# Optimization experiments

Measured on AMD Instinct MI355X. Metric: run time of the kernel, lower is better.

Reference implementation:

```python
import jax, jax.numpy as jnp
import numpy as np

V = 131072          # total vertices (hits) across all events
K = 64              # neighbours per vertex, col 0 == self
NSEG = 4            # number of events (row splits segments)
THRESHOLD = 0.5     # hierarchy score cut (layer's non-trainable threshold var)


def setup_inputs() -> dict:
    key = jax.random.key(0)
    k1, k2 = jax.random.split(key)
    score = jax.random.uniform(k1, (V, 1), dtype=jnp.float32)
    seg = V // NSEG
    base = (jnp.arange(V, dtype=jnp.int32) // seg) * seg
    # random neighbours constrained to the same segment; column 0 is self
    rnd = jax.random.randint(k2, (V, K - 1), 0, seg, dtype=jnp.int32) + base[:, None]
    nidxs = jnp.concatenate([jnp.arange(V, dtype=jnp.int32)[:, None], rnd], axis=1)
    row_splits = (jnp.arange(NSEG + 1, dtype=jnp.int32) * seg)
    return {"score": score, "nidxs": nidxs, "row_splits": row_splits}


def _local_group(score1, nidxs, row_splits, thr):
    """Greedy threshold-based neighbour grouping (HGCalML LocalGroup op).

    Vertices are visited per segment in descending score order. An unused
    vertex becomes a group seed; if its score > thr it absorbs all of its
    not-yet-used neighbours. Returns fixed-shape (-1 padded) outputs so the
    whole thing is jit-compatible.
    """
    V_, K_ = nidxs.shape
    seg_id = jnp.searchsorted(row_splits, jnp.arange(V_, dtype=row_splits.dtype),
                              side='right') - 1
    # per-segment descending-score order == tf.argsort(DESC) per row split
    order = jnp.lexsort((-score1, seg_id)).astype(jnp.int32)
    kcols = jnp.arange(K_)

    def step(state, v):
        used, assign, dirn, sel, seed, count = state
        is_new = jnp.logical_not(used[v])                 # v not grouped yet -> seed
        expand = score1[v] > thr                          # absorb neighbours?
        cand = jnp.where(expand, nidxs[v],
                         jnp.where(kcols == 0, v, -1))    # else only self
        safe = jnp.clip(cand, 0, V_ - 1)
        valid = (cand >= 0) & jnp.logical_not(used[safe]) & is_new
        used = used.at[safe].set(used[safe] | valid)
        assign = assign.at[safe].set(jnp.where(valid, count, assign[safe]))
        dirn = dirn.at[v].set(jnp.where(valid, cand, -1))
        sel = sel.at[count].set(jnp.where(is_new, v, sel[count]))
        seed = seed.at[v].set(seed[v] | is_new)
        count = count + is_new.astype(jnp.int32)
        return (used, assign, dirn, sel, seed, count), None

    init = (jnp.zeros(V_, dtype=bool),                 # used
            jnp.full(V_, -1, jnp.int32),               # backgather: seed rank per vertex
            jnp.full((V_, K_), -1, jnp.int32),         # directed neighbour idxs
            jnp.full(V_, -1, jnp.int32),               # selected seed vertices, -1 padded
            jnp.zeros(V_, dtype=bool),                 # seed mask
            jnp.int32(0))
    (used, assign, dirn, sel, seed, count), _ = jax.lax.scan(step, init, order)
    cs0 = jnp.concatenate([jnp.zeros(1, jnp.int32),
                           jnp.cumsum(seed.astype(jnp.int32))])
    rs_new = cs0[row_splits]                           # new row splits over seeds
    return rs_new, dirn, sel[:, None], assign, count


def reference(score, nidxs, row_splits):
    # layer: score = clip(score, 0, 1); per-segment argsort; LocalGroup
    score1 = jnp.clip(score.reshape(-1), 0.0, 1.0)
    rs_new, dirnidx, sel, backgather, n_sel = _local_group(score1, nidxs,
                                                           row_splits, THRESHOLD)
    # return_backscatter=True -> back = [V, sel]; we return sel (padded) + n_sel
    # outputs: directed nidx (V,K), selection idxs (V,1 padded with -1),
    #          backgather (V,), new row splits, number selected
    return dirnidx, sel, backgather, rs_new, n_sel
```

## Files before the change

kernel.cpp:

```cpp
#include <hip/hip_runtime.h>
#include <stdint.h>

#define INFU 0xFFFFFFFFu
#define LCAP 32768
#define NC 128

__global__ void __launch_bounds__(256) k_hist(const float* score, unsigned* bcnt,
                                              unsigned* claim, int* sel, int V, int SEGN){
  int v = blockIdx.x*blockDim.x+threadIdx.x; if (v>=V) return;
  claim[v]=INFU;
  sel[v]=-1;
  float s = score[v]; s = fminf(fmaxf(s,0.f),1.f);
  int b = (int)(s*(float)SEGN); if (b>=SEGN) b=SEGN-1; if (b<0) b=0;
  int bd = SEGN-1-b;
  int seg = v / SEGN;
  atomicAdd(&bcnt[(size_t)seg*SEGN+bd], 1u);
}

__global__ void __launch_bounds__(1024) k_scan(const unsigned* in, const unsigned* claim,
                                               unsigned* outExcl, unsigned* segTotal,
                                               int SEGN, int mode){
  int seg = blockIdx.x; int tid = threadIdx.x; int lane = tid&63, wv = tid>>6;
  __shared__ unsigned wsum[16];
  const int CH = (SEGN+1023)>>10;
  int i0 = tid*CH, i1 = i0+CH; if (i1>SEGN) i1=SEGN;
  const size_t base = (size_t)seg*SEGN;
  unsigned sum=0;
  for (int i=i0;i<i1;i++){
    unsigned x = (mode==0)? in[base+i] : ((claim[base+i]==INFU)?1u:0u);
    sum+=x;
  }
  unsigned incl=sum;
  for (int off=1;off<64;off<<=1){ unsigned t=__shfl_up(incl,(unsigned)off); if (lane>=off) incl+=t; }
  if (lane==63) wsum[wv]=incl;
  __syncthreads();
  unsigned wbase=0,total=0;
  for (int w=0;w<16;w++){ unsigned s=wsum[w]; if (w<wv) wbase+=s; total+=s; }
  unsigned run = wbase + incl - sum;
  for (int i=i0;i<i1;i++){
    unsigned x = (mode==0)? in[base+i] : ((claim[base+i]==INFU)?1u:0u);
    outExcl[base+i]=run; run+=x;
  }
  if (tid==0 && segTotal) segTotal[seg]=total;
}

__global__ void __launch_bounds__(256) k_scatter(const float* score, const unsigned* bbase,
                                                 unsigned* bfill, unsigned long long* slot,
                                                 int V, int SEGN){
  int v = blockIdx.x*blockDim.x+threadIdx.x; if (v>=V) return;
  float s = score[v]; s=fminf(fmaxf(s,0.f),1.f);
  int b=(int)(s*(float)SEGN); if(b>=SEGN)b=SEGN-1; if(b<0)b=0;
  int bd=SEGN-1-b; int seg=v/SEGN;
  size_t bk = (size_t)seg*SEGN+bd;
  unsigned pos = bbase[bk] + atomicAdd(&bfill[bk],1u);
  unsigned kb = ~__float_as_uint(s);
  slot[(size_t)seg*SEGN+pos] = ((unsigned long long)kb<<32) | (unsigned)v;
}

__global__ void __launch_bounds__(256) k_bsort(const unsigned* bcnt, const unsigned* bbase,
                                               unsigned long long* slot, int V, int SEGN){
  int t = blockIdx.x*blockDim.x+threadIdx.x; if (t>=V) return;
  unsigned n = bcnt[t];
  if (n<2) return;
  int seg = t / SEGN;
  unsigned long long* a = slot + (size_t)seg*SEGN + bbase[t];
  for (unsigned i=1;i<n;i++){
    unsigned long long key=a[i]; int j=(int)i-1;
    while (j>=0 && a[j]>key){ a[j+1]=a[j]; j--; }
    a[j+1]=key;
  }
}

__global__ void __launch_bounds__(256) k_build(const unsigned long long* slot,
                                               int* ord, unsigned* rnkv, int* segE,
                                               int V, int SEGN){
  int r = blockIdx.x*blockDim.x+threadIdx.x; if (r>=V) return;
  unsigned long long sl = slot[r];
  int v = (int)(unsigned)(sl & 0xFFFFFFFFull);
  ord[r]=v;
  int seg = r / SEGN; int rl = r - seg*SEGN;
  rnkv[v] = (unsigned)rl;
  float s = __uint_as_float(~(unsigned)(sl>>32));
  bool ex = (s > 0.5f);
  if (rl==0 && !ex) segE[seg]=0;
  if (ex){
    if (rl==SEGN-1) segE[seg]=SEGN;
    else {
      float s2 = __uint_as_float(~(unsigned)(slot[r+1]>>32));
      if (!(s2 > 0.5f)) segE[seg]=rl+1;
    }
  }
}

__global__ void __launch_bounds__(256) k_pack4(const int* ord, const unsigned* rnkv, const int* nidxs,
                                               const int* segE, unsigned short* nbr16,
                                               int V, int K, int SEGN){
  const int K4 = K>>2;
  long long q = (long long)blockIdx.x*256 + threadIdx.x;
  if (q >= (long long)V*K4) return;
  int gr = (int)(q / K4); int k4 = (int)(q - (long long)gr*K4);
  int seg = gr / SEGN, r = gr - seg*SEGN;
  if (r >= segE[seg]) return;
  int v = ord[gr];
  const int4 nn = *(const int4*)(nidxs + (size_t)v*K + (size_t)k4*4);
  ushort4 o;
  o.x=(unsigned short)rnkv[nn.x]; o.y=(unsigned short)rnkv[nn.y];
  o.z=(unsigned short)rnkv[nn.z]; o.w=(unsigned short)rnkv[nn.w];
  *(ushort4*)(nbr16 + (size_t)gr*K + (size_t)k4*4) = o;
}
__global__ void __launch_bounds__(256) k_pack(const int* ord, const unsigned* rnkv, const int* nidxs,
                                              const int* segE, unsigned short* nbr16,
                                              int V, int K, int SEGN){
  long long t = (long long)blockIdx.x*256 + threadIdx.x;
  if (t >= (long long)V*K) return;
  int gr = (int)(t / K); int k = (int)(t - (long long)gr*K);
  int seg = gr / SEGN, r = gr - seg*SEGN;
  if (r >= segE[seg]) return;
  int v = ord[gr];
  int w = nidxs[(size_t)v*K + k];
  nbr16[t] = (unsigned short)rnkv[w];
}

__global__ void __launch_bounds__(1024) k_greedy(const unsigned short* nbr16, const int* ord,
                                                 const int* segE,
                                                 unsigned* claim, unsigned* srank,
                                                 unsigned* segTotal, unsigned* absorb,
                                                 int SEGN, int K){
  __shared__ unsigned s_cl[LCAP/2];
  __shared__ unsigned char s_pos[LCAP];
  __shared__ unsigned s_cand[NC];
  __shared__ unsigned long long s_McLo[NC];
  __shared__ unsigned long long s_McHi[NC];
  __shared__ unsigned long long s_anyLo, s_anyHi;
  __shared__ unsigned long long s_bm[16];
  __shared__ unsigned s_ws[16];
  __shared__ unsigned s_base;
  __shared__ unsigned s_wcur;
  __shared__ unsigned long long s_v0, s_v1;
  const int seg = blockIdx.x, tid = threadIdx.x, lane = tid&63, wv = tid>>6;
  unsigned* clg = claim + (size_t)seg*SEGN;
  const size_t segbase = (size_t)seg*SEGN;
  const int E = segE[seg];
  const int cap = (LCAP < SEGN) ? LCAP : SEGN;
  const int capw = (cap+1)>>1;
  for (int i=tid; i<capw; i+=1024) s_cl[i]=0xFFFFFFFFu;
  for (int i=tid; i<((cap+3)>>2); i+=1024) ((unsigned*)s_pos)[i]=0u;
  if (tid<NC) s_cand[tid]=INFU;
  const unsigned long long lt_mask = (lane==0) ? 0ull : ((~0ull) >> (64-lane));
  unsigned wcursor = 0;
  for (;;){
    __syncthreads();
    if (tid<NC){
      unsigned pc = s_cand[tid];
      if (pc!=INFU && pc<(unsigned)cap) s_pos[pc]=0;
      s_cand[tid]=INFU; s_McLo[tid]=0ull; s_McHi[tid]=0ull;
    }
    if (tid==NC)   s_anyLo=0ull;
    if (tid==NC+1) s_anyHi=0ull;
    int found = 0;
    for (;;){
      unsigned r = wcursor + (unsigned)(wv*64 + lane);
      bool undec=false;
      if (r<(unsigned)E){
        if (r<(unsigned)cap)
          undec = (((s_cl[r>>1]>>((r&1)*16))&0xFFFFu)==0xFFFFu);
        else
          undec = (__hip_atomic_load(&clg[r], __ATOMIC_RELAXED, __HIP_MEMORY_SCOPE_AGENT)==INFU);
      }
      unsigned long long m = __ballot(undec);
      if (lane==0) s_bm[wv]=m;
      __syncthreads();
      unsigned long long mb = (lane<16)? s_bm[lane] : 0ull;
      int pc16 = (int)__popcll(mb);
      int incl = pc16;
      #pragma unroll
      for (int off=1; off<16; off<<=1){ int t=__shfl_up(incl,off); if (lane>=off) incl+=t; }
      int total = __shfl(incl, 15);
      int below = __shfl(incl, wv) - __shfl(pc16, wv);
      int pos = found + below + (int)__popcll(m & lt_mask);
      if (undec && pos<NC){
        s_cand[pos]=r;
        if (r<(unsigned)cap) s_pos[r]=(unsigned char)(pos+1);
      }
      if (undec && pos==NC-1) s_wcur=r+1;
      bool filled = (found+total>=NC);
      bool winend = (wcursor + 1024 >= (unsigned)E);
      __syncthreads();
      if (filled){ wcursor = s_wcur; found=NC; break; }
      found += total;
      if (winend){ wcursor=(unsigned)E; break; }
      wcursor += 1024;
    }
    const int ncand = found;
    if (!ncand) break;
    unsigned rwq[8], cq[8];
    #pragma unroll
    for (int q=0;q<8;q++){
      int c=(wv<<3)|q;
      cq[q] = (c<ncand) ? s_cand[c] : INFU;
    }
    #pragma unroll
    for (int q=0;q<8;q++){
      rwq[q]=INFU;
      if (cq[q]!=INFU && lane<K)
        rwq[q] = (unsigned)nbr16[(segbase + cq[q])*K + lane];
    }
    const bool fastmap = (s_cand[ncand-1] < (unsigned)cap);
    #pragma unroll
    for (int q=0;q<8;q++){
      int c=(wv<<3)|q;
      if (cq[q]!=INFU){
        unsigned rw = rwq[q];
        int p = -1;
        if (fastmap){
          if (rw<(unsigned)cap){ p = (int)s_pos[rw] - 1; }
        } else {
          int pp=0;
          if (s_cand[pp+64]<=rw) pp+=64;
          if (s_cand[pp+32]<=rw) pp+=32;
          if (s_cand[pp+16]<=rw) pp+=16;
          if (s_cand[pp+8 ]<=rw) pp+=8;
          if (s_cand[pp+4 ]<=rw) pp+=4;
          if (s_cand[pp+2 ]<=rw) pp+=2;
          if (s_cand[pp+1 ]<=rw) pp+=1;
          if (pp<ncand && s_cand[pp]==rw) p=pp;
        }
        if (lane<K && p>c){
          if (p<64){ atomicOr(&s_McLo[c], 1ull<<p);      atomicOr(&s_anyLo, 1ull<<p); }
          else     { atomicOr(&s_McHi[c], 1ull<<(p-64)); atomicOr(&s_anyHi, 1ull<<(p-64)); }
        }
      }
    }
    __syncthreads();
    if (wv==0){
      const int n0 = (ncand<64)? ncand : 64;
      const int n1 = ncand - n0;
      const unsigned long long nmask0 = (n0==64)? ~0ull : ((1ull<<n0)-1ull);
      unsigned long long Mj0 = s_McLo[lane];
      unsigned long long any0 = s_anyLo & nmask0;
      unsigned long long valid0 = (~any0) & nmask0;
      unsigned long long rem = any0;
      while (rem){
        int i=__builtin_ctzll(rem); rem &= rem-1;
        bool pred = ((valid0>>lane)&1ull) && (lane<i) && ((Mj0>>i)&1ull);
        if (__ballot(pred)==0ull) valid0 |= (1ull<<i);
      }
      unsigned long long valid1 = 0ull;
      if (n1>0){
        const unsigned long long nmask1 = (n1==64)? ~0ull : ((1ull<<n1)-1ull);
        unsigned long long sp = ((valid0>>lane)&1ull) ? s_McHi[lane] : 0ull;
        #pragma unroll
        for (int off=32; off; off>>=1)
          sp |= (unsigned long long)__shfl_xor((long long)sp, off);
        unsigned long long Mj1 = s_McHi[64+lane];
        unsigned long long any1 = s_anyHi & nmask1;
        valid1 = (~(any1|sp)) & nmask1;
        unsigned long long rem1 = any1 & ~sp;
        while (rem1){
          int i=__builtin_ctzll(rem1); rem1 &= rem1-1;
          bool pred = ((valid1>>lane)&1ull) && (lane<i) && ((Mj1>>i)&1ull);
          if (__ballot(pred)==0ull) valid1 |= (1ull<<i);
        }
      }
      if (lane==0){ s_v0=valid0; s_v1=valid1; }
    }
    __syncthreads();
    const unsigned long long v0 = s_v0, v1 = s_v1;
    #pragma unroll
    for (int q=0;q<8;q++){
      int c=(wv<<3)|q;
      bool isv = (c<64) ? (((v0>>c)&1ull)!=0ull) : (((v1>>(c-64))&1ull)!=0ull);
      if (cq[q]!=INFU && isv){
        unsigned rw=rwq[q], cr=cq[q];
        if (rw>cr && rw!=INFU){
          if (rw<(unsigned)cap){
            unsigned idx=rw>>1, sh=(rw&1)*16;
            unsigned old=s_cl[idx];
            for(;;){
              unsigned curv=(old>>sh)&0xFFFFu;
              if (cr>=curv) break;
              unsigned neu=(old & ~(0xFFFFu<<sh)) | (cr<<sh);
              unsigned prev=atomicCAS(&s_cl[idx], old, neu);
              if (prev==old) break;
              old=prev;
            }
          } else {
            atomicMin(&clg[rw], cr);
          }
        }
      }
    }
  }
  __syncthreads();
  if (cap == SEGN){
    if (tid==0) s_base=0;
    __syncthreads();
    for (int p=0; p<cap; p+=1024){
      int i = p + tid;
      bool live = (i<cap);
      unsigned c16 = 0xFFFFu;
      if (live) c16 = (s_cl[i>>1]>>((i&1)*16))&0xFFFFu;
      bool isSeed = live && (c16==0xFFFFu);
      unsigned long long m = __ballot(isSeed);
      if (lane==0) s_ws[wv]=(unsigned)__popcll(m);
      __syncthreads();
      unsigned wbase=0, tot=0;
      for (int w2=0;w2<16;w2++){ unsigned t2=s_ws[w2]; if (w2<wv) wbase+=t2; tot+=t2; }
      unsigned ex = s_base + wbase + (unsigned)__popcll(m & lt_mask);
      if (live){
        srank[segbase + i] = ex;
        clg[i] = isSeed ? INFU : c16;
        absorb[ord[segbase + i]] = isSeed ? (unsigned)i : c16;
      }
      __syncthreads();
      if (tid==0) s_base += tot;
    }
    __syncthreads();
    if (tid==0) segTotal[seg] = s_base;
  } else {
    for (int r=tid; r<cap; r+=1024){
      unsigned c=(s_cl[r>>1]>>((r&1)*16))&0xFFFFu;
      clg[r] = (c==0xFFFFu) ? INFU : c;
    }
  }
}

__global__ void __launch_bounds__(256) k_absorb(const unsigned* rnkv, const unsigned* claim,
                                                unsigned* absorb, int V, int SEGN){
  int v = blockIdx.x*blockDim.x+threadIdx.x; if (v>=V) return;
  int seg = v / SEGN;
  unsigned r = rnkv[v];
  unsigned c = claim[(size_t)seg*SEGN + r];
  absorb[v] = (c==INFU)? r : c;
}

__global__ void __launch_bounds__(256) k_dirnAll4(const int* nidxs, const unsigned* rnkv,
                                                  const unsigned* absorb, const float* score,
                                                  const unsigned* segTotal,
                                                  const unsigned* srank,
                                                  int* dirn, int* sel, int* backg,
                                                  int* rs, int* nsel,
                                                  int V, int K, int SEGN, int NSEG){
  const int K4 = K>>2;
  long long q = (long long)blockIdx.x*256 + threadIdx.x;
  if (q >= (long long)V*K4) return;
  int v = (int)(q / K4); int k4 = (int)(q - (long long)v*K4);
  int seg = v / SEGN;
  if (q <= (long long)NSEG){
    unsigned run=0;
    for (int s=0;s<(int)q;s++) run+=segTotal[s];
    rs[q]=(int)run;
    if ((int)q==NSEG) nsel[0]=(int)run;
  }
  unsigned r = rnkv[v];
  unsigned a_self = absorb[v];
  bool seed = (a_self == r);
  if (k4==0){
    unsigned segOff=0;
    for (int s=0;s<seg;s++) segOff+=segTotal[s];
    unsigned g = segOff + srank[(size_t)seg*SEGN + a_self];
    backg[v] = (int)g;
    if (seed) sel[g] = v;
  }
  int4 o = make_int4(-1,-1,-1,-1);
  if (seed){
    float s = score[v]; s=fminf(fmaxf(s,0.f),1.f);
    if (!(s > 0.5f)){
      if (k4==0) o.x = v;
    } else {
      const int4 nn = *(const int4*)(nidxs + (size_t)v*K + (size_t)k4*4);
      if (absorb[nn.x]==r) o.x=nn.x;
      if (absorb[nn.y]==r) o.y=nn.y;
      if (absorb[nn.z]==r) o.z=nn.z;
      if (absorb[nn.w]==r) o.w=nn.w;
    }
  }
  *(int4*)(dirn + (size_t)v*K + (size_t)k4*4) = o;
}
__global__ void __launch_bounds__(256) k_dirnAll(const int* nidxs, const unsigned* rnkv,
                                                 const unsigned* absorb, const float* score,
                                                 const unsigned* segTotal,
                                                 const unsigned* srank,
                                                 int* dirn, int* sel, int* backg,
                                                 int* rs, int* nsel,
                                                 int V, int K, int SEGN, int NSEG){
  long long t = (long long)blockIdx.x*blockDim.x + threadIdx.x;
  if (t >= (long long)V*K) return;
  int v = (int)(t / K); int j = (int)(t - (long long)v*K);
  int seg = v / SEGN;
  if (t <= (long long)NSEG){
    unsigned run=0;
    for (int s=0;s<(int)t;s++) run+=segTotal[s];
    rs[t]=(int)run;
    if ((int)t==NSEG) nsel[0]=(int)run;
  }
  unsigned r = rnkv[v];
  unsigned a_self = absorb[v];
  bool seed = (a_self == r);
  if (j==0){
    unsigned segOff=0;
    for (int s=0;s<seg;s++) segOff+=segTotal[s];
    unsigned g = segOff + srank[(size_t)seg*SEGN + a_self];
    backg[v] = (int)g;
    if (seed) sel[g] = v;
  }
  int out = -1;
  if (seed){
    float s = score[v]; s=fminf(fmaxf(s,0.f),1.f);
    if (!(s > 0.5f)){
      out = (j==0)? v : -1;
    } else {
      int w = nidxs[(size_t)v*K + j];
      out = (absorb[w] == r)? w : -1;
    }
  }
  dirn[t] = out;
}

extern "C" void kernel_launch(void* const* d_in, const int* in_sizes, int n_in,
                              void* d_out, int out_size, void* d_ws, size_t ws_size,
                              hipStream_t stream) {
  const float* score   = (const float*)d_in[0];
  const int*   nidxs   = (const int*)d_in[1];
  (void)d_in[2];

  const int V    = in_sizes[0];
  const int K    = in_sizes[1] / V;
  const int NSEG = in_sizes[2] - 1;
  const int SEGN = V / NSEG;

  char* w = (char*)d_ws;
  unsigned long long* slot = (unsigned long long*)w;  w += (size_t)V*8;
  unsigned* bcnt  = (unsigned*)w; w += (size_t)V*4;
  unsigned* bfill = (unsigned*)w; w += (size_t)V*4;
  unsigned* bbase = (unsigned*)w; w += (size_t)V*4;
  int*      ord   = (int*)w;      w += (size_t)V*4;
  unsigned* rnkv  = (unsigned*)w; w += (size_t)V*4;
  unsigned* claim = (unsigned*)w; w += (size_t)V*4;
  unsigned* srank = (unsigned*)w; w += (size_t)V*4;
  unsigned* segTotal = (unsigned*)w; w += 64;
  int*      segE     = (int*)w;      w += 64;
  unsigned* absorb = bcnt;

  int* out      = (int*)d_out;
  int* out_dirn = out;
  int* out_sel  = out + (size_t)V*K;
  int* out_bg   = out_sel + V;
  int* out_rs   = out_bg + V;
  int* out_nsel = out_rs + (NSEG+1);

  unsigned short* nbr16 = (unsigned short*)out_dirn;

  hipMemsetAsync(bcnt,  0x00, (size_t)V*8, stream);

  int nb256 = (V + 255)/256;
  long long totVK = (long long)V*K;
  int nbVK = (int)((totVK + 255)/256);
  const bool vec4 = (K>=4) && ((K&3)==0);
  int nbQ = (int)(((long long)V*(K>>2) + 255)/256);

  k_hist<<<nb256, 256, 0, stream>>>(score, bcnt, claim, out_sel, V, SEGN);
  k_scan<<<NSEG, 1024, 0, stream>>>(bcnt, nullptr, bbase, nullptr, SEGN, 0);
  k_scatter<<<nb256, 256, 0, stream>>>(score, bbase, bfill, slot, V, SEGN);
  k_bsort<<<nb256, 256, 0, stream>>>(bcnt, bbase, slot, V, SEGN);
  k_build<<<nb256, 256, 0, stream>>>(slot, ord, rnkv, segE, V, SEGN);
  if (vec4) k_pack4<<<nbQ, 256, 0, stream>>>(ord, rnkv, nidxs, segE, nbr16, V, K, SEGN);
  else      k_pack <<<nbVK, 256, 0, stream>>>(ord, rnkv, nidxs, segE, nbr16, V, K, SEGN);
  k_greedy<<<NSEG, 1024, 0, stream>>>(nbr16, ord, segE, claim, srank, segTotal, absorb,
                                      SEGN, K);
  if (SEGN > LCAP){
    k_scan<<<NSEG, 1024, 0, stream>>>(nullptr, claim, srank, segTotal, SEGN, 1);
    k_absorb<<<nb256, 256, 0, stream>>>(rnkv, claim, absorb, V, SEGN);
  }
  if (vec4) k_dirnAll4<<<nbQ, 256, 0, stream>>>(nidxs, rnkv, absorb, score, segTotal, srank,
                                                out_dirn, out_sel, out_bg, out_rs, out_nsel,
                                                V, K, SEGN, NSEG);
  else      k_dirnAll<<<nbVK, 256, 0, stream>>>(nidxs, rnkv, absorb, score, segTotal, srank,
                                                out_dirn, out_sel, out_bg, out_rs, out_nsel,
                                                V, K, SEGN, NSEG);
}
```

Baseline: 327.1 us.

## Fuse bucket sort with order build, parallelise scans, count threshold via histogram

```diff
diff --git a/kernel.cpp b/kernel.cpp
--- a/kernel.cpp
+++ b/kernel.cpp
@@ -6,15 +6,68 @@
 #define NC 128
 
 __global__ void __launch_bounds__(256) k_hist(const float* score, unsigned* bcnt,
-                                              unsigned* claim, int* sel, int V, int SEGN){
+                                              unsigned* claim, int* sel, unsigned* segE,
+                                              int V, int SEGN, int initClaim){
   int v = blockIdx.x*blockDim.x+threadIdx.x; if (v>=V) return;
-  claim[v]=INFU;
+  if (initClaim) claim[v]=INFU;
   sel[v]=-1;
   float s = score[v]; s = fminf(fmaxf(s,0.f),1.f);
+  int seg = v / SEGN;
+  bool ex = (s > 0.5f);
+  unsigned long long act = __ballot(true);
+  unsigned long long mex = __ballot(ex);
+  int lane = threadIdx.x & 63;
+  int seg0 = __shfl(seg, 0);
+  bool uni = (act == ~0ull) && (__shfl(seg,63) == seg0);
+  if (uni){
+    if (lane==0 && mex) atomicAdd(&segE[seg0], (unsigned)__popcll(mex));
+  } else {
+    if (ex) atomicAdd(&segE[seg], 1u);
+  }
   int b = (int)(s*(float)SEGN); if (b>=SEGN) b=SEGN-1; if (b<0) b=0;
   int bd = SEGN-1-b;
-  int seg = v / SEGN;
   atomicAdd(&bcnt[(size_t)seg*SEGN+bd], 1u);
+}
+
+__global__ void __launch_bounds__(1024) k_scan0(const unsigned* bcnt, unsigned* bbase,
+                                                unsigned* bfill, int SEGN){
+  int seg = blockIdx.x; int tid = threadIdx.x; int lane = tid&63, wv = tid>>6;
+  __shared__ unsigned s_wc[1024];
+  const size_t base = (size_t)seg*SEGN;
+  const int NP = (SEGN+1023)>>10;
+  for (int p=0;p<NP;p++){
+    int i = p*1024 + tid;
+    unsigned x = (i<SEGN)? bcnt[base+i] : 0u;
+    unsigned incl = x;
+    #pragma unroll
+    for (int off=1;off<64;off<<=1){ unsigned t=__shfl_up(incl,(unsigned)off); if (lane>=off) incl+=t; }
+    if (lane==63) s_wc[p*16+wv]=incl;
+  }
+  __syncthreads();
+  if (wv==0){
+    unsigned carry=0; int n=NP*16;
+    for (int ch=0; ch*64<n; ch++){
+      int idx=ch*64+lane;
+      unsigned x=(idx<n)? s_wc[idx]:0u;
+      unsigned incl=x;
+      #pragma unroll
+      for (int off=1;off<64;off<<=1){ unsigned t=__shfl_up(incl,(unsigned)off); if (lane>=off) incl+=t; }
+      if (idx<n) s_wc[idx]=carry+incl-x;
+      carry += __shfl(incl,63);
+    }
+  }
+  __syncthreads();
+  for (int p=0;p<NP;p++){
+    int i = p*1024 + tid;
+    if (i<SEGN){
+      unsigned x = bcnt[base+i];
+      unsigned incl = x;
+      #pragma unroll
+      for (int off=1;off<64;off<<=1){ unsigned t=__shfl_up(incl,(unsigned)off); if (lane>=off) incl+=t; }
+      bbase[base+i] = s_wc[p*16+wv] + incl - x;
+      bfill[base+i] = 0u;
+    }
+  }
 }
 
 __global__ void __launch_bounds__(1024) k_scan(const unsigned* in, const unsigned* claim,
@@ -57,50 +110,38 @@
   slot[(size_t)seg*SEGN+pos] = ((unsigned long long)kb<<32) | (unsigned)v;
 }
 
-__global__ void __launch_bounds__(256) k_bsort(const unsigned* bcnt, const unsigned* bbase,
-                                               unsigned long long* slot, int V, int SEGN){
+__global__ void __launch_bounds__(256) k_bsortbuild(const unsigned* bcnt, const unsigned* bbase,
+                                                    unsigned long long* slot,
+                                                    int* ord, unsigned* rnkv,
+                                                    int V, int SEGN){
   int t = blockIdx.x*blockDim.x+threadIdx.x; if (t>=V) return;
   unsigned n = bcnt[t];
-  if (n<2) return;
+  if (!n) return;
   int seg = t / SEGN;
-  unsigned long long* a = slot + (size_t)seg*SEGN + bbase[t];
+  const size_t segbase = (size_t)seg*SEGN;
+  unsigned base = bbase[t];
+  unsigned long long* a = slot + segbase + base;
   for (unsigned i=1;i<n;i++){
     unsigned long long key=a[i]; int j=(int)i-1;
     while (j>=0 && a[j]>key){ a[j+1]=a[j]; j--; }
     a[j+1]=key;
   }
-}
-
-__global__ void __launch_bounds__(256) k_build(const unsigned long long* slot,
-                                               int* ord, unsigned* rnkv, int* segE,
-                                               int V, int SEGN){
-  int r = blockIdx.x*blockDim.x+threadIdx.x; if (r>=V) return;
-  unsigned long long sl = slot[r];
-  int v = (int)(unsigned)(sl & 0xFFFFFFFFull);
-  ord[r]=v;
-  int seg = r / SEGN; int rl = r - seg*SEGN;
-  rnkv[v] = (unsigned)rl;
-  float s = __uint_as_float(~(unsigned)(sl>>32));
-  bool ex = (s > 0.5f);
-  if (rl==0 && !ex) segE[seg]=0;
-  if (ex){
-    if (rl==SEGN-1) segE[seg]=SEGN;
-    else {
-      float s2 = __uint_as_float(~(unsigned)(slot[r+1]>>32));
-      if (!(s2 > 0.5f)) segE[seg]=rl+1;
-    }
+  for (unsigned i=0;i<n;i++){
+    int v = (int)(unsigned)(a[i] & 0xFFFFFFFFull);
+    ord[segbase + base + i] = v;
+    rnkv[v] = base + i;
   }
 }
 
 __global__ void __launch_bounds__(256) k_pack4(const int* ord, const unsigned* rnkv, const int* nidxs,
-                                               const int* segE, unsigned short* nbr16,
+                                               const unsigned* segE, unsigned short* nbr16,
                                                int V, int K, int SEGN){
   const int K4 = K>>2;
   long long q = (long long)blockIdx.x*256 + threadIdx.x;
   if (q >= (long long)V*K4) return;
   int gr = (int)(q / K4); int k4 = (int)(q - (long long)gr*K4);
   int seg = gr / SEGN, r = gr - seg*SEGN;
-  if (r >= segE[seg]) return;
+  if (r >= (int)segE[seg]) return;
   int v = ord[gr];
   const int4 nn = *(const int4*)(nidxs + (size_t)v*K + (size_t)k4*4);
   ushort4 o;
@@ -109,20 +150,20 @@
   *(ushort4*)(nbr16 + (size_t)gr*K + (size_t)k4*4) = o;
 }
 __global__ void __launch_bounds__(256) k_pack(const int* ord, const unsigned* rnkv, const int* nidxs,
-                                              const int* segE, unsigned short* nbr16,
+                                              const unsigned* segE, unsigned short* nbr16,
                                               int V, int K, int SEGN){
   long long t = (long long)blockIdx.x*256 + threadIdx.x;
   if (t >= (long long)V*K) return;
   int gr = (int)(t / K); int k = (int)(t - (long long)gr*K);
   int seg = gr / SEGN, r = gr - seg*SEGN;
-  if (r >= segE[seg]) return;
+  if (r >= (int)segE[seg]) return;
   int v = ord[gr];
   int w = nidxs[(size_t)v*K + k];
   nbr16[t] = (unsigned short)rnkv[w];
 }
 
 __global__ void __launch_bounds__(1024) k_greedy(const unsigned short* nbr16, const int* ord,
-                                                 const int* segE,
+                                                 const unsigned* segEp,
                                                  unsigned* claim, unsigned* srank,
                                                  unsigned* segTotal, unsigned* absorb,
                                                  int SEGN, int K){
@@ -133,14 +174,13 @@
   __shared__ unsigned long long s_McHi[NC];
   __shared__ unsigned long long s_anyLo, s_anyHi;
   __shared__ unsigned long long s_bm[16];
-  __shared__ unsigned s_ws[16];
   __shared__ unsigned s_base;
   __shared__ unsigned s_wcur;
   __shared__ unsigned long long s_v0, s_v1;
   const int seg = blockIdx.x, tid = threadIdx.x, lane = tid&63, wv = tid>>6;
   unsigned* clg = claim + (size_t)seg*SEGN;
   const size_t segbase = (size_t)seg*SEGN;
-  const int E = segE[seg];
+  const int E = (int)segEp[seg];
   const int cap = (LCAP < SEGN) ? LCAP : SEGN;
   const int capw = (cap+1)>>1;
   for (int i=tid; i<capw; i+=1024) s_cl[i]=0xFFFFFFFFu;
@@ -293,29 +333,41 @@
   }
   __syncthreads();
   if (cap == SEGN){
-    if (tid==0) s_base=0;
+    unsigned* s_wc = (unsigned*)s_pos;
+    const int NP = (cap+1023)>>10;
+    for (int p=0;p<NP;p++){
+      int i = p*1024 + tid;
+      bool isSeed=false;
+      if (i<cap) isSeed = (((s_cl[i>>1]>>((i&1)*16))&0xFFFFu)==0xFFFFu);
+      unsigned long long m = __ballot(isSeed);
+      if (lane==0) s_wc[p*16+wv]=(unsigned)__popcll(m);
+    }
     __syncthreads();
-    for (int p=0; p<cap; p+=1024){
-      int i = p + tid;
-      bool live = (i<cap);
-      unsigned c16 = 0xFFFFu;
-      if (live) c16 = (s_cl[i>>1]>>((i&1)*16))&0xFFFFu;
-      bool isSeed = live && (c16==0xFFFFu);
-      unsigned long long m = __ballot(isSeed);
-      if (lane==0) s_ws[wv]=(unsigned)__popcll(m);
-      __syncthreads();
-      unsigned wbase=0, tot=0;
-      for (int w2=0;w2<16;w2++){ unsigned t2=s_ws[w2]; if (w2<wv) wbase+=t2; tot+=t2; }
-      unsigned ex = s_base + wbase + (unsigned)__popcll(m & lt_mask);
-      if (live){
+    if (wv==0){
+      unsigned carry=0; int n=NP*16;
+      for (int ch=0; ch*64<n; ch++){
+        int idx=ch*64+lane;
+        unsigned x=(idx<n)? s_wc[idx]:0u;
+        unsigned incl=x;
+        #pragma unroll
+        for (int off=1;off<64;off<<=1){ unsigned t2=__shfl_up(incl,(unsigned)off); if (lane>=off) incl+=t2; }
+        if (idx<n) s_wc[idx]=carry+incl-x;
+        carry += __shfl(incl,63);
+      }
+      if (lane==0) s_base=carry;
+    }
+    __syncthreads();
+    for (int p=0;p<NP;p++){
+      int i = p*1024 + tid;
+      if (i<cap){
+        unsigned c16=(s_cl[i>>1]>>((i&1)*16))&0xFFFFu;
+        bool isSeed=(c16==0xFFFFu);
+        unsigned long long m = __ballot(isSeed);
+        unsigned ex = s_wc[p*16+wv] + (unsigned)__popcll(m & lt_mask);
         srank[segbase + i] = ex;
-        clg[i] = isSeed ? INFU : c16;
-        absorb[ord[segbase + i]] = isSeed ? (unsigned)i : c16;
-      }
-      __syncthreads();
-      if (tid==0) s_base += tot;
-    }
-    __syncthreads();
+        absorb[ord[segbase + i]] = isSeed ? (unsigned)i : (unsigned)c16;
+      }
+    }
     if (tid==0) segTotal[seg] = s_base;
   } else {
     for (int r=tid; r<cap; r+=1024){
@@ -432,6 +484,7 @@
   char* w = (char*)d_ws;
   unsigned long long* slot = (unsigned long long*)w;  w += (size_t)V*8;
   unsigned* bcnt  = (unsigned*)w; w += (size_t)V*4;
+  unsigned* segE  = (unsigned*)w; w += 64;
   unsigned* bfill = (unsigned*)w; w += (size_t)V*4;
   unsigned* bbase = (unsigned*)w; w += (size_t)V*4;
   int*      ord   = (int*)w;      w += (size_t)V*4;
@@ -439,7 +492,6 @@
   unsigned* claim = (unsigned*)w; w += (size_t)V*4;
   unsigned* srank = (unsigned*)w; w += (size_t)V*4;
   unsigned* segTotal = (unsigned*)w; w += 64;
-  int*      segE     = (int*)w;      w += 64;
   unsigned* absorb = bcnt;
 
   int* out      = (int*)d_out;
@@ -451,19 +503,19 @@
 
   unsigned short* nbr16 = (unsigned short*)out_dirn;
 
-  hipMemsetAsync(bcnt,  0x00, (size_t)V*8, stream);
+  hipMemsetAsync(bcnt, 0x00, (size_t)V*4 + 64, stream);
 
   int nb256 = (V + 255)/256;
   long long totVK = (long long)V*K;
   int nbVK = (int)((totVK + 255)/256);
   const bool vec4 = (K>=4) && ((K&3)==0);
   int nbQ = (int)(((long long)V*(K>>2) + 255)/256);
-
-  k_hist<<<nb256, 256, 0, stream>>>(score, bcnt, claim, out_sel, V, SEGN);
-  k_scan<<<NSEG, 1024, 0, stream>>>(bcnt, nullptr, bbase, nullptr, SEGN, 0);
+  const int initClaim = (SEGN > LCAP) ? 1 : 0;
+
+  k_hist<<<nb256, 256, 0, stream>>>(score, bcnt, claim, out_sel, segE, V, SEGN, initClaim);
+  k_scan0<<<NSEG, 1024, 0, stream>>>(bcnt, bbase, bfill, SEGN);
   k_scatter<<<nb256, 256, 0, stream>>>(score, bbase, bfill, slot, V, SEGN);
-  k_bsort<<<nb256, 256, 0, stream>>>(bcnt, bbase, slot, V, SEGN);
-  k_build<<<nb256, 256, 0, stream>>>(slot, ord, rnkv, segE, V, SEGN);
+  k_bsortbuild<<<nb256, 256, 0, stream>>>(bcnt, bbase, slot, ord, rnkv, V, SEGN);
   if (vec4) k_pack4<<<nbQ, 256, 0, stream>>>(ord, rnkv, nidxs, segE, nbr16, V, K, SEGN);
   else      k_pack <<<nbVK, 256, 0, stream>>>(ord, rnkv, nidxs, segE, nbr16, V, K, SEGN);
   k_greedy<<<NSEG, 1024, 0, stream>>>(nbr16, ord, segE, claim, srank, segTotal, absorb,
```

Result: no change. 329.7 us (+0.8%).
